# Performance work log

Hardware: AMD Instinct MI355X
Metric: run time of the kernel (lower is better)

## Reference

```python
import jax, jax.numpy as jnp
import numpy as np

S, B, D, H, K, M, MEM = 1024, 2, 1024, 16, 64, 4096, 1
T = (MEM + 1) * S  # key length = (mem_len+1)*seq_len


def setup_inputs() -> dict:
    key = jax.random.key(0)
    ks = jax.random.split(key, 16)

    def w(k, shape):  # N(0, 0.02) init as in the torch module
        return jax.random.normal(k, shape, dtype=jnp.float32) * 0.02

    x = jax.random.normal(ks[0], (S, B, D), dtype=jnp.float32)
    p = jax.random.normal(ks[1], (T, B, D), dtype=jnp.float32)
    memory = jax.random.normal(ks[2], (MEM * S, B, D), dtype=jnp.float32)
    u_bias = w(ks[3], (H, K))
    v_bias = w(ks[4], (H, K))
    # Transformer-XL causal mask: query s may attend to keys t <= mem_len*S + s
    t_idx = jnp.arange(T)[None, :]
    s_idx = jnp.arange(S)[:, None]
    mask = jnp.where(t_idx <= MEM * S + s_idx, 0.0, -1e9).astype(jnp.float32)[None]  # [1,S,T]
    return {
        "x": x, "p": p, "mask": mask, "memory": memory,
        "u_bias": u_bias, "v_bias": v_bias,
        "wq_w": w(ks[5], (H * K, D)), "wke_w": w(ks[6], (H * K, D)),
        "wkr_w": w(ks[7], (H * K, D)), "wv_w": w(ks[8], (H * K, D)),
        "wc_w": w(ks[9], (D, H * K)),
        "w1_w": w(ks[10], (M, D)), "w1_b": jnp.zeros((M,), jnp.float32),
        "w2_w": w(ks[11], (D, M)), "w2_b": jnp.zeros((D,), jnp.float32),
        "ln1_g": jnp.ones((D,), jnp.float32), "ln1_b": jnp.zeros((D,), jnp.float32),
        "ln2_g": jnp.ones((D,), jnp.float32), "ln2_b": jnp.zeros((D,), jnp.float32),
    }


def _layernorm(x, g, b, eps=1e-5):
    mu = jnp.mean(x, axis=-1, keepdims=True)
    var = jnp.mean(jnp.square(x - mu), axis=-1, keepdims=True)
    return (x - mu) / jnp.sqrt(var + eps) * g + b


def reference(x, p, mask, memory, u_bias, v_bias,
              wq_w, wke_w, wkr_w, wv_w, wc_w,
              w1_w, w1_b, w2_w, w2_b, ln1_g, ln1_b, ln2_g, ln2_b):
    s_len, b_sz, d = x.shape
    q = (x @ wq_w.T).reshape(s_len, b_sz, H, K)            # [S,B,H,K]
    x_mem = jnp.concatenate([memory, x], axis=0)           # [T,B,D]
    k_e = (x_mem @ wke_w.T).reshape(T, b_sz, H, K)         # content keys
    k_r = (p @ wkr_w.T).reshape(T, b_sz, H, K)             # relative-position keys
    v = (x_mem @ wv_w.T).reshape(T, b_sz, H, K)
    # AC: content score, BD: relative-position score (Transformer-XL)
    ac = jnp.einsum("sbhk,tbhk->bhst", q + u_bias, k_e)
    bd = jnp.einsum("sbhk,tbhk->bhst", q + v_bias, k_r)
    alpha = (ac + bd) / np.sqrt(K).astype(np.float32) + mask[:, None]  # [B,H,S,T]
    alpha = jax.nn.softmax(alpha, axis=-1)
    av = jnp.einsum("bhst,tbhk->sbhk", alpha, v).reshape(s_len, b_sz, H * K)
    u = av @ wc_w.T
    u = _layernorm(u + x, ln1_g, ln1_b)
    z = jax.nn.relu(u @ w1_w.T + w1_b) @ w2_w.T + w2_b
    z = _layernorm(z + u, ln2_g, ln2_b)
    return z
```

## Files before the change

kernel.cpp:

```cpp
#include <hip/hip_runtime.h>
#include <math.h>

#define S_LEN 1024
#define BATCH 2
#define DM 1024
#define NH 16
#define HD 64
#define FFN_DIM 4096
#define T_LEN 2048
#define RQ 2048
#define RT 4096
#define KROW 72
#define NPART 2

typedef __attribute__((ext_vector_type(8))) short short8;
typedef __attribute__((ext_vector_type(4))) float f32x4;

__device__ __forceinline__ unsigned short f2bf(float f) {
    unsigned u = __builtin_bit_cast(unsigned, f);
    u += 0x7fffu + ((u >> 16) & 1u);
    return (unsigned short)(u >> 16);
}
__device__ __forceinline__ float bf2f(unsigned short s) { return __builtin_bit_cast(float, ((unsigned)s) << 16); }

#define GLD_LDS16(gptr, lptr)                                                                  \
    __builtin_amdgcn_global_load_lds((const __attribute__((address_space(1))) unsigned int*)(gptr), \
                                     (__attribute__((address_space(3))) unsigned int*)(lptr), 16, 0, 0)

__device__ __forceinline__ ushort4 cvt4(float4 v) {
    ushort4 o;
    o.x = f2bf(v.x); o.y = f2bf(v.y); o.z = f2bf(v.z); o.w = f2bf(v.w);
    return o;
}

__global__ void cast_all_kernel(const float* __restrict__ wq, const float* __restrict__ wke,
                                const float* __restrict__ wv, const float* __restrict__ wkr,
                                const float* __restrict__ wc, const float* __restrict__ w1,
                                const float* __restrict__ w2, const float* __restrict__ x,
                                const float* __restrict__ p, const float* __restrict__ mem,
                                unsigned short* __restrict__ wdst, unsigned short* __restrict__ xbf,
                                unsigned short* __restrict__ pbf, unsigned short* __restrict__ xm) {
    const long Q = 256 * 1024;
    const long W = 13 * Q;
    long i = (long)blockIdx.x * blockDim.x + threadIdx.x;
    if (i < W) {
        const float* src; long off;
        if      (i < 1 * Q) { src = wq;  off = 0; }
        else if (i < 2 * Q) { src = wke; off = 1 * Q; }
        else if (i < 3 * Q) { src = wv;  off = 2 * Q; }
        else if (i < 4 * Q) { src = wkr; off = 3 * Q; }
        else if (i < 5 * Q) { src = wc;  off = 4 * Q; }
        else if (i < 9 * Q) { src = w1;  off = 5 * Q; }
        else                { src = w2;  off = 9 * Q; }
        ((ushort4*)wdst)[i] = cvt4(((const float4*)src)[i - off]);
    } else if (i < W + 2 * Q) {
        long j = i - W;
        ((ushort4*)xbf)[j] = cvt4(((const float4*)x)[j]);
    } else if (i < W + 6 * Q) {
        long j = i - W - 2 * Q;
        ((ushort4*)pbf)[j] = cvt4(((const float4*)p)[j]);
    } else {
        long j = i - W - 6 * Q;
        float4 v = (j < 2 * Q) ? ((const float4*)mem)[j] : ((const float4*)x)[j - 2 * Q];
        ((ushort4*)xm)[j] = cvt4(v);
    }
}

#define BM 128
#define BN 128
#define BK 32

__launch_bounds__(256)
__global__ void proj_fused(const unsigned short* __restrict__ xbf, const unsigned short* __restrict__ xmbf,
                           const unsigned short* __restrict__ pbf, const unsigned short* __restrict__ wqb,
                           const unsigned short* __restrict__ wkevb, const unsigned short* __restrict__ wkrb,
                           unsigned short* __restrict__ qo, unsigned short* __restrict__ keo,
                           unsigned short* __restrict__ vTo, unsigned short* __restrict__ kro) {
    __shared__ __align__(16) short As[BM * BK];
    __shared__ __align__(16) short Bs[BN * BK];
    const int id = blockIdx.x;
    const unsigned short *A, *B;
    unsigned short *Yb, *Yv = nullptr;
    int bx, by;
    if (id < 128)      { A = xbf;  B = wqb;   Yb = qo;  bx = id & 7;   by = id >> 3; }
    else if (id < 640) { int t = id - 128; A = xmbf; B = wkevb; Yb = keo; Yv = vTo;
                         bx = t & 15; by = t >> 4; }
    else               { int t = id - 640; A = pbf;  B = wkrb;  Yb = kro;
                         bx = t & 7;  by = t >> 3; }
    const int tid = threadIdx.x;
    const int w = tid >> 6, lane = tid & 63;
    const int row0 = by * BM, col0 = bx * BN;
    const int wr = (w >> 1) * 64, wcn = (w & 1) * 64;
    f32x4 acc[4][4] = {};
    const int lrow = lane & 15, quad = lane >> 4;
    for (int k0 = 0; k0 < DM; k0 += BK) {
        __syncthreads();
#pragma unroll
        for (int i = 0; i < 2; ++i) {
            int c = w * 128 + i * 64 + lane;
            int row = c >> 2, kg = c & 3;
            int kl = (kg - (row >> 1)) & 3;
            GLD_LDS16(A + (long)(row0 + row) * DM + k0 + kl * 8, As + (w * 128 + i * 64) * 8);
            GLD_LDS16(B + (long)(col0 + row) * DM + k0 + kl * 8, Bs + (w * 128 + i * 64) * 8);
        }
        __syncthreads();
        short8 a[4], b[4];
#pragma unroll
        for (int mi = 0; mi < 4; ++mi) {
            int r = wr + mi * 16 + lrow;
            int ph = (quad + (r >> 1)) & 3;
            a[mi] = *(const short8*)&As[r * BK + ph * 8];
        }
#pragma unroll
        for (int ni = 0; ni < 4; ++ni) {
            int r = wcn + ni * 16 + lrow;
            int ph = (quad + (r >> 1)) & 3;
            b[ni] = *(const short8*)&Bs[r * BK + ph * 8];
        }
#pragma unroll
        for (int mi = 0; mi < 4; ++mi)
#pragma unroll
            for (int ni = 0; ni < 4; ++ni)
                acc[mi][ni] = __builtin_amdgcn_mfma_f32_16x16x32_bf16(a[mi], b[ni], acc[mi][ni], 0, 0, 0);
    }
    const int mb = row0 + wr + quad * 4;
    const int nb = col0 + wcn + lrow;
    const bool isv = (Yv != nullptr) && (col0 >= 1024);
#pragma unroll
    for (int mi = 0; mi < 4; ++mi)
#pragma unroll
        for (int ni = 0; ni < 4; ++ni) {
            const int r = mb + mi * 16, cc = nb + ni * 16;
#pragma unroll
            for (int reg = 0; reg < 4; ++reg) {
                float val = acc[mi][ni][reg];
                const int rf = r + reg;
                if (isv) {
                    int c2 = cc - 1024;
                    int t = rf >> 1, b2 = rf & 1;
                    int h2 = c2 >> 6, d2 = c2 & 63;
                    Yv[((long)(b2 * NH + h2) * HD + d2) * T_LEN + t] = f2bf(val);
                } else {
                    Yb[(long)rf * DM + cc] = f2bf(val);
                }
            }
        }
}

__launch_bounds__(256)
__global__ void gemm_mfma(const unsigned short* __restrict__ A, const unsigned short* __restrict__ B,
                          const float* __restrict__ bias, float* __restrict__ Yf,
                          unsigned short* __restrict__ Yb, int Kd, int N, int relu,
                          int klen, long pstride) {
    __shared__ __align__(16) short As[BM * BK];
    __shared__ __align__(16) short Bs[BN * BK];
    const int tid = threadIdx.x;
    const int w = tid >> 6, lane = tid & 63;
    const int row0 = blockIdx.y * BM, col0 = blockIdx.x * BN;
    const int kbeg = blockIdx.z * klen;
    const int wr = (w >> 1) * 64, wcn = (w & 1) * 64;
    f32x4 acc[4][4] = {};
    const int lrow = lane & 15, quad = lane >> 4;
    for (int k0 = kbeg; k0 < kbeg + klen; k0 += BK) {
        __syncthreads();
#pragma unroll
        for (int i = 0; i < 2; ++i) {
            int c = w * 128 + i * 64 + lane;
            int row = c >> 2, kg = c & 3;
            int kl = (kg - (row >> 1)) & 3;
            GLD_LDS16(A + (long)(row0 + row) * Kd + k0 + kl * 8, As + (w * 128 + i * 64) * 8);
            GLD_LDS16(B + (long)(col0 + row) * Kd + k0 + kl * 8, Bs + (w * 128 + i * 64) * 8);
        }
        __syncthreads();
        short8 a[4], b[4];
#pragma unroll
        for (int mi = 0; mi < 4; ++mi) {
            int r = wr + mi * 16 + lrow;
            int ph = (quad + (r >> 1)) & 3;
            a[mi] = *(const short8*)&As[r * BK + ph * 8];
        }
#pragma unroll
        for (int ni = 0; ni < 4; ++ni) {
            int r = wcn + ni * 16 + lrow;
            int ph = (quad + (r >> 1)) & 3;
            b[ni] = *(const short8*)&Bs[r * BK + ph * 8];
        }
#pragma unroll
        for (int mi = 0; mi < 4; ++mi)
#pragma unroll
            for (int ni = 0; ni < 4; ++ni)
                acc[mi][ni] = __builtin_amdgcn_mfma_f32_16x16x32_bf16(a[mi], b[ni], acc[mi][ni], 0, 0, 0);
    }
    const int mb = row0 + wr + quad * 4;
    const int nb = col0 + wcn + lrow;
    float* of = Yf ? Yf + (long)blockIdx.z * pstride : nullptr;
    float bb[4];
#pragma unroll
    for (int ni = 0; ni < 4; ++ni) bb[ni] = bias ? bias[nb + ni * 16] : 0.f;
#pragma unroll
    for (int mi = 0; mi < 4; ++mi)
#pragma unroll
        for (int ni = 0; ni < 4; ++ni) {
            const int r = mb + mi * 16, cc = nb + ni * 16;
#pragma unroll
            for (int reg = 0; reg < 4; ++reg) {
                float val = acc[mi][ni][reg] + bb[ni];
                if (relu) val = fmaxf(val, 0.f);
                if (Yb) Yb[(long)(r + reg) * N + cc] = f2bf(val);
                else    of[(long)(r + reg) * N + cc] = val;
            }
        }
}

__launch_bounds__(256)
__global__ void prep_kernel(const unsigned short* __restrict__ kr,
                            const float* __restrict__ ub, const float* __restrict__ vb,
                            unsigned short* __restrict__ ke_io, float* __restrict__ biasg) {
    const int r = blockIdx.x;
    const int tid = threadIdx.x;
    const int h = tid >> 4, seg = tid & 15;
    ushort4 keu = ((const ushort4*)(ke_io + (long)r * DM))[tid];
    ushort4 kru = ((const ushort4*)(kr + (long)r * DM))[tid];
    float ke0 = bf2f(keu.x), ke1 = bf2f(keu.y), ke2 = bf2f(keu.z), ke3 = bf2f(keu.w);
    float kr0 = bf2f(kru.x), kr1 = bf2f(kru.y), kr2 = bf2f(kru.z), kr3 = bf2f(kru.w);
    float4 u4 = ((const float4*)ub)[tid];
    float4 v4 = ((const float4*)vb)[tid];
    ushort4 s;
    s.x = f2bf((ke0 + kr0) * 0.125f); s.y = f2bf((ke1 + kr1) * 0.125f);
    s.z = f2bf((ke2 + kr2) * 0.125f); s.w = f2bf((ke3 + kr3) * 0.125f);
    ((ushort4*)(ke_io + (long)r * DM))[tid] = s;
    float part = u4.x * ke0 + u4.y * ke1 + u4.z * ke2 + u4.w * ke3
               + v4.x * kr0 + v4.y * kr1 + v4.z * kr2 + v4.w * kr3;
    part += __shfl_xor(part, 1);
    part += __shfl_xor(part, 2);
    part += __shfl_xor(part, 4);
    part += __shfl_xor(part, 8);
    if (seg == 0) {
        const int t = r >> 1, b = r & 1;
        biasg[(b * NH + h) * T_LEN + t] = part * 0.125f;
    }
}

__launch_bounds__(256)
__global__ void attn_mfma(const unsigned short* __restrict__ qg,
                          const unsigned short* __restrict__ ksum,
                          const unsigned short* __restrict__ vT,
                          const float* __restrict__ biasg,
                          float* __restrict__ Opart, float2* __restrict__ mlout) {
    __shared__ __align__(16) unsigned short Ks[64 * KROW];
    __shared__ __align__(16) unsigned short Vs[64 * KROW];
    __shared__ __align__(16) unsigned short Ps[4][16 * KROW];
    const int bid = blockIdx.x;
    const int part = bid >> 9, rid = bid & 511;
    const int stile = rid & 15, h = (rid >> 4) & 15, b = rid >> 8;
    const int tid = threadIdx.x, w = tid >> 6, lane = tid & 63;
    const int L = lane & 15, quad = lane >> 4;
    const int qbase = stile * 64 + w * 16;
    short8 qf0, qf1;
    {
        const unsigned short* qp = qg + ((long)(qbase + L) * 2 + b) * DM + h * HD + quad * 8;
        qf0 = *(const short8*)(qp);
        qf1 = *(const short8*)(qp + 32);
    }
    f32x4 O[4] = {};
    float mrow[4] = {-1e30f, -1e30f, -1e30f, -1e30f};
    float lrow[4] = {0.f, 0.f, 0.f, 0.f};
    const int nch = 17 + stile;
    const float* bias_p = biasg + (long)(b * NH + h) * T_LEN;
    const unsigned short* ks_base = ksum + (long)b * DM + h * HD;
    const unsigned short* vt_base = vT + (long)(b * NH + h) * HD * T_LEN;
    const int c0 = tid, c1 = 256 + tid;
    const int row_a = c0 >> 3, seg_a = c0 & 7;
    const int row_b = c1 >> 3, seg_b = c1 & 7;
    uint4 pk0, pk1, pv0, pv1;
    {
        const int tf = part * 64;
        pk0 = *(const uint4*)(ks_base + (long)(tf + row_a) * 2 * DM + seg_a * 8);
        pk1 = *(const uint4*)(ks_base + (long)(tf + row_b) * 2 * DM + seg_b * 8);
        pv0 = *(const uint4*)(vt_base + (long)row_a * T_LEN + tf + seg_a * 8);
        pv1 = *(const uint4*)(vt_base + (long)row_b * T_LEN + tf + seg_b * 8);
    }
    for (int ch = part; ch < nch; ch += NPART) {
        const int t0 = ch * 64;
        __syncthreads();
        *(uint4*)&Ks[row_a * KROW + seg_a * 8] = pk0;
        *(uint4*)&Ks[row_b * KROW + seg_b * 8] = pk1;
        *(uint4*)&Vs[row_a * KROW + seg_a * 8] = pv0;
        *(uint4*)&Vs[row_b * KROW + seg_b * 8] = pv1;
        __syncthreads();
        if (ch + NPART < nch) {
            const int t1 = t0 + NPART * 64;
            pk0 = *(const uint4*)(ks_base + (long)(t1 + row_a) * 2 * DM + seg_a * 8);
            pk1 = *(const uint4*)(ks_base + (long)(t1 + row_b) * 2 * DM + seg_b * 8);
            pv0 = *(const uint4*)(vt_base + (long)row_a * T_LEN + t1 + seg_a * 8);
            pv1 = *(const uint4*)(vt_base + (long)row_b * T_LEN + t1 + seg_b * 8);
        }
        f32x4 S[4] = {};
#pragma unroll
        for (int kt = 0; kt < 4; ++kt) {
            short8 kb0 = *(const short8*)&Ks[(kt * 16 + L) * KROW + quad * 8];
            short8 kb1 = *(const short8*)&Ks[(kt * 16 + L) * KROW + 32 + quad * 8];
            S[kt] = __builtin_amdgcn_mfma_f32_16x16x32_bf16(qf0, kb0, S[kt], 0, 0, 0);
            S[kt] = __builtin_amdgcn_mfma_f32_16x16x32_bf16(qf1, kb1, S[kt], 0, 0, 0);
        }
        float sc[4][4];
        float cm[4] = {-1e30f, -1e30f, -1e30f, -1e30f};
#pragma unroll
        for (int kt = 0; kt < 4; ++kt) {
            float bt = bias_p[t0 + kt * 16 + L];
#pragma unroll
            for (int reg = 0; reg < 4; ++reg) {
                float v = S[kt][reg] + bt;
                if (t0 + kt * 16 + L > 1024 + qbase + quad * 4 + reg) v = -1e30f;
                sc[kt][reg] = v;
                cm[reg] = fmaxf(cm[reg], v);
            }
        }
#pragma unroll
        for (int off = 1; off < 16; off <<= 1)
#pragma unroll
            for (int reg = 0; reg < 4; ++reg) cm[reg] = fmaxf(cm[reg], __shfl_xor(cm[reg], off));
        float cf[4];
#pragma unroll
        for (int reg = 0; reg < 4; ++reg) {
            float mn = fmaxf(mrow[reg], cm[reg]);
            cf[reg] = __expf(mrow[reg] - mn);
            mrow[reg] = mn;
            lrow[reg] *= cf[reg];
        }
        float rs[4] = {0.f, 0.f, 0.f, 0.f};
#pragma unroll
        for (int kt = 0; kt < 4; ++kt)
#pragma unroll
            for (int reg = 0; reg < 4; ++reg) {
                float pv = __expf(sc[kt][reg] - mrow[reg]);
                rs[reg] += pv;
                Ps[w][(quad * 4 + reg) * KROW + kt * 16 + L] = f2bf(pv);
            }
#pragma unroll
        for (int off = 1; off < 16; off <<= 1)
#pragma unroll
            for (int reg = 0; reg < 4; ++reg) rs[reg] += __shfl_xor(rs[reg], off);
#pragma unroll
        for (int reg = 0; reg < 4; ++reg) lrow[reg] += rs[reg];
#pragma unroll
        for (int dt = 0; dt < 4; ++dt)
#pragma unroll
            for (int reg = 0; reg < 4; ++reg) O[dt][reg] *= cf[reg];
        short8 pa0 = *(const short8*)&Ps[w][L * KROW + quad * 8];
        short8 pa1 = *(const short8*)&Ps[w][L * KROW + 32 + quad * 8];
#pragma unroll
        for (int dt = 0; dt < 4; ++dt) {
            short8 vb0 = *(const short8*)&Vs[(dt * 16 + L) * KROW + quad * 8];
            short8 vb1 = *(const short8*)&Vs[(dt * 16 + L) * KROW + 32 + quad * 8];
            O[dt] = __builtin_amdgcn_mfma_f32_16x16x32_bf16(pa0, vb0, O[dt], 0, 0, 0);
            O[dt] = __builtin_amdgcn_mfma_f32_16x16x32_bf16(pa1, vb1, O[dt], 0, 0, 0);
        }
    }
    const long rbase = ((long)(part * 2 + b) * NH + h) * S_LEN;
#pragma unroll
    for (int reg = 0; reg < 4; ++reg) {
        const int s = qbase + quad * 4 + reg;
        float* op = Opart + (rbase + s) * 64;
#pragma unroll
        for (int dt = 0; dt < 4; ++dt) op[dt * 16 + L] = O[dt][reg];
        if (L == 0) mlout[rbase + s] = make_float2(mrow[reg], lrow[reg]);
    }
}

__launch_bounds__(256)
__global__ void attn_combine(const float* __restrict__ Opart, const float2* __restrict__ ml,
                             unsigned short* __restrict__ avout) {
    const int i = blockIdx.x * 256 + threadIdx.x;
    const int d4 = i & 15;
    const int row = i >> 4;
    const int s = row & 1023;
    const int bh = row >> 10;
    const int b = bh >> 4, h = bh & 15;
    float2 ml0 = ml[row], ml1 = ml[row + 32768];
    float m = fmaxf(ml0.x, ml1.x);
    float a0 = __expf(ml0.x - m), a1 = __expf(ml1.x - m);
    float inv = 1.f / (a0 * ml0.y + a1 * ml1.y);
    a0 *= inv; a1 *= inv;
    float4 o0 = ((const float4*)Opart)[(long)row * 16 + d4];
    float4 o1 = ((const float4*)Opart)[((long)row + 32768) * 16 + d4];
    float4 o;
    o.x = a0 * o0.x + a1 * o1.x;
    o.y = a0 * o0.y + a1 * o1.y;
    o.z = a0 * o0.z + a1 * o1.z;
    o.w = a0 * o0.w + a1 * o1.w;
    *(ushort4*)(avout + ((long)s * 2 + b) * DM + h * HD + d4 * 4) = cvt4(o);
}

__launch_bounds__(256)
__global__ void ln_kernel(const float* __restrict__ a0, const float* __restrict__ a1,
                          const float* __restrict__ cb, const float* __restrict__ r,
                          const float* __restrict__ g, const float* __restrict__ be,
                          float* __restrict__ out, unsigned short* __restrict__ outb) {
    const int row = blockIdx.x;
    const int tid = threadIdx.x;
    float4 xa = ((const float4*)(a0 + (long)row * DM))[tid];
    if (a1) {
        float4 x1 = ((const float4*)(a1 + (long)row * DM))[tid];
        xa.x += x1.x; xa.y += x1.y; xa.z += x1.z; xa.w += x1.w;
    }
    if (cb) {
        float4 c4 = ((const float4*)cb)[tid];
        xa.x += c4.x; xa.y += c4.y; xa.z += c4.z; xa.w += c4.w;
    }
    float4 xr = ((const float4*)(r + (long)row * DM))[tid];
    float4 x = make_float4(xa.x + xr.x, xa.y + xr.y, xa.z + xr.z, xa.w + xr.w);
    float s1 = x.x + x.y + x.z + x.w;
    float s2 = x.x * x.x + x.y * x.y + x.z * x.z + x.w * x.w;
#pragma unroll
    for (int off = 32; off > 0; off >>= 1) {
        s1 += __shfl_down(s1, off);
        s2 += __shfl_down(s2, off);
    }
    __shared__ float w1s[4], w2s[4];
    const int wid = tid >> 6;
    if ((tid & 63) == 0) { w1s[wid] = s1; w2s[wid] = s2; }
    __syncthreads();
    float S1 = w1s[0] + w1s[1] + w1s[2] + w1s[3];
    float S2 = w2s[0] + w2s[1] + w2s[2] + w2s[3];
    float mu = S1 * (1.f / 1024.f);
    float var = S2 * (1.f / 1024.f) - mu * mu;
    float rstd = rsqrtf(var + 1e-5f);
    float4 gv = ((const float4*)g)[tid];
    float4 bv = ((const float4*)be)[tid];
    float4 o;
    o.x = (x.x - mu) * rstd * gv.x + bv.x;
    o.y = (x.y - mu) * rstd * gv.y + bv.y;
    o.z = (x.z - mu) * rstd * gv.z + bv.z;
    o.w = (x.w - mu) * rstd * gv.w + bv.w;
    ((float4*)(out + (long)row * DM))[tid] = o;
    if (outb) ((ushort4*)(outb + (long)row * DM))[tid] = cvt4(o);
}

extern "C" void kernel_launch(void* const* d_in, const int* in_sizes, int n_in,
                              void* d_out, int out_size, void* d_ws, size_t ws_size,
                              hipStream_t stream) {
    (void)in_sizes; (void)n_in; (void)out_size; (void)ws_size;
    const float* x    = (const float*)d_in[0];
    const float* p    = (const float*)d_in[1];
    const float* mem  = (const float*)d_in[3];
    const float* ub   = (const float*)d_in[4];
    const float* vb   = (const float*)d_in[5];
    const float* wq   = (const float*)d_in[6];
    const float* wke  = (const float*)d_in[7];
    const float* wkr  = (const float*)d_in[8];
    const float* wv   = (const float*)d_in[9];
    const float* wc   = (const float*)d_in[10];
    const float* w1   = (const float*)d_in[11];
    const float* w1b  = (const float*)d_in[12];
    const float* w2   = (const float*)d_in[13];
    const float* w2b  = (const float*)d_in[14];
    const float* ln1g = (const float*)d_in[15];
    const float* ln1b = (const float*)d_in[16];
    const float* ln2g = (const float*)d_in[17];
    const float* ln2b = (const float*)d_in[18];
    float* out = (float*)d_out;
    float* wsf = (float*)d_ws;
    unsigned short* ws16 = (unsigned short*)d_ws;

    const long HLF = 512 * 1024;
    const long M16 = 1024 * 1024;
    unsigned short* wq_bf   = ws16 + 0 * M16;
    unsigned short* wkev_bf = ws16 + 1 * M16;
    unsigned short* wkr_bf  = ws16 + 3 * M16;
    unsigned short* wc_bf   = ws16 + 4 * M16;
    unsigned short* w1_bf   = ws16 + 5 * M16;
    unsigned short* w2_bf   = ws16 + 9 * M16;
    unsigned short* x_bf   = (unsigned short*)(wsf + 13 * HLF);
    unsigned short* xm_bf  = (unsigned short*)(wsf + 15 * HLF);
    unsigned short* p_bf   = (unsigned short*)(wsf + 19 * HLF);
    unsigned short* q_bf   = (unsigned short*)(wsf + 23 * HLF);
    unsigned short* ke_bf  = (unsigned short*)(wsf + 25 * HLF);
    unsigned short* kr_bf  = (unsigned short*)(wsf + 29 * HLF);
    unsigned short* vT_bf  = (unsigned short*)(wsf + 33 * HLF);
    float* abias           = wsf + 37 * HLF;
    float* Opart           = wsf + 15 * HLF;
    float2* mlpart         = (float2*)(wsf + 29 * HLF);
    unsigned short* avb_bf = (unsigned short*)(wsf + 13 * HLF);
    float* t1p             = wsf + 15 * HLF;
    float* u               = wsf + 25 * HLF;
    unsigned short* u_bf   = (unsigned short*)(wsf + 23 * HLF);
    unsigned short* z1_bf  = (unsigned short*)(wsf + 15 * HLF);
    float* t2p             = wsf + 29 * HLF;
    const long PSTR = (long)2048 * 1024;

    cast_all_kernel<<<23552, 256, 0, stream>>>(wq, wke, wv, wkr, wc, w1, w2, x, p, mem,
                                               ws16, x_bf, p_bf, xm_bf);
    proj_fused<<<896, 256, 0, stream>>>(x_bf, xm_bf, p_bf, wq_bf, wkev_bf, wkr_bf,
                                        q_bf, ke_bf, vT_bf, kr_bf);
    prep_kernel<<<RT, 256, 0, stream>>>(kr_bf, ub, vb, ke_bf, abias);
    attn_mfma<<<512 * NPART, 256, 0, stream>>>(q_bf, ke_bf, vT_bf, abias, Opart, mlpart);
    attn_combine<<<2048, 256, 0, stream>>>(Opart, mlpart, avb_bf);
    gemm_mfma<<<dim3(8, 16, 2), 256, 0, stream>>>(avb_bf, wc_bf, nullptr, t1p, nullptr,
                                                  DM, DM, 0, 512, PSTR);
    ln_kernel<<<RQ, 256, 0, stream>>>(t1p, t1p + PSTR, nullptr, x, ln1g, ln1b, u, u_bf);
    gemm_mfma<<<dim3(32, 16, 1), 256, 0, stream>>>(u_bf, w1_bf, w1b, nullptr, z1_bf,
                                                   DM, FFN_DIM, 1, DM, 0);
    gemm_mfma<<<dim3(8, 16, 2), 256, 0, stream>>>(z1_bf, w2_bf, nullptr, t2p, nullptr,
                                                  FFN_DIM, DM, 0, 2048, PSTR);
    ln_kernel<<<RQ, 256, 0, stream>>>(t2p, t2p + PSTR, w2b, u, ln2g, ln2b, out, nullptr);
}
```

Baseline: 406.8 us.

## Split attention key range three ways, prefetch bias, mask only final chunk

The attention kernel now splits each query tile's key chunks across three partitions instead of two, launching more blocks to improve GPU fill and load balance across the causal-length tiles. The combine kernel merges three partial softmax results, and workspace buffers are re-laid out so the extra partial output fits. The per-chunk bias load is prefetched one iteration ahead together with K/V, and the causal mask compare runs only on the diagonal chunk. In exchange, the extra partition writes and reads more partial output and adds one more exp and rescale per row in the combine step.

Result: no change. 402.3 us (-1.1%).

```diff
diff --git a/kernel.cpp b/kernel.cpp
--- a/kernel.cpp
+++ b/kernel.cpp
@@ -11,7 +11,8 @@
 #define RQ 2048
 #define RT 4096
 #define KROW 72
-#define NPART 2
+#define NPART 3
+#define OPSTR 2097152L
 
 typedef __attribute__((ext_vector_type(8))) short short8;
 typedef __attribute__((ext_vector_type(4))) float f32x4;
@@ -246,7 +247,8 @@
                           const unsigned short* __restrict__ ksum,
                           const unsigned short* __restrict__ vT,
                           const float* __restrict__ biasg,
-                          float* __restrict__ Opart, float2* __restrict__ mlout) {
+                          float* __restrict__ Op01, float* __restrict__ Op2,
+                          float2* __restrict__ mlout) {
     __shared__ __align__(16) unsigned short Ks[64 * KROW];
     __shared__ __align__(16) unsigned short Vs[64 * KROW];
     __shared__ __align__(16) unsigned short Ps[4][16 * KROW];
@@ -273,12 +275,15 @@
     const int row_a = c0 >> 3, seg_a = c0 & 7;
     const int row_b = c1 >> 3, seg_b = c1 & 7;
     uint4 pk0, pk1, pv0, pv1;
+    float pb[4];
     {
         const int tf = part * 64;
         pk0 = *(const uint4*)(ks_base + (long)(tf + row_a) * 2 * DM + seg_a * 8);
         pk1 = *(const uint4*)(ks_base + (long)(tf + row_b) * 2 * DM + seg_b * 8);
         pv0 = *(const uint4*)(vt_base + (long)row_a * T_LEN + tf + seg_a * 8);
         pv1 = *(const uint4*)(vt_base + (long)row_b * T_LEN + tf + seg_b * 8);
+#pragma unroll
+        for (int kt = 0; kt < 4; ++kt) pb[kt] = bias_p[tf + kt * 16 + L];
     }
     for (int ch = part; ch < nch; ch += NPART) {
         const int t0 = ch * 64;
@@ -288,12 +293,16 @@
         *(uint4*)&Vs[row_a * KROW + seg_a * 8] = pv0;
         *(uint4*)&Vs[row_b * KROW + seg_b * 8] = pv1;
         __syncthreads();
-        if (ch + NPART < nch) {
+        const bool more = (ch + NPART < nch);
+        float pbn[4];
+        if (more) {
             const int t1 = t0 + NPART * 64;
             pk0 = *(const uint4*)(ks_base + (long)(t1 + row_a) * 2 * DM + seg_a * 8);
             pk1 = *(const uint4*)(ks_base + (long)(t1 + row_b) * 2 * DM + seg_b * 8);
             pv0 = *(const uint4*)(vt_base + (long)row_a * T_LEN + t1 + seg_a * 8);
             pv1 = *(const uint4*)(vt_base + (long)row_b * T_LEN + t1 + seg_b * 8);
+#pragma unroll
+            for (int kt = 0; kt < 4; ++kt) pbn[kt] = bias_p[t1 + kt * 16 + L];
         }
         f32x4 S[4] = {};
 #pragma unroll
@@ -305,16 +314,25 @@
         }
         float sc[4][4];
         float cm[4] = {-1e30f, -1e30f, -1e30f, -1e30f};
-#pragma unroll
-        for (int kt = 0; kt < 4; ++kt) {
-            float bt = bias_p[t0 + kt * 16 + L];
-#pragma unroll
-            for (int reg = 0; reg < 4; ++reg) {
-                float v = S[kt][reg] + bt;
-                if (t0 + kt * 16 + L > 1024 + qbase + quad * 4 + reg) v = -1e30f;
-                sc[kt][reg] = v;
-                cm[reg] = fmaxf(cm[reg], v);
-            }
+        if (ch != nch - 1) {
+#pragma unroll
+            for (int kt = 0; kt < 4; ++kt)
+#pragma unroll
+                for (int reg = 0; reg < 4; ++reg) {
+                    float v = S[kt][reg] + pb[kt];
+                    sc[kt][reg] = v;
+                    cm[reg] = fmaxf(cm[reg], v);
+                }
+        } else {
+#pragma unroll
+            for (int kt = 0; kt < 4; ++kt)
+#pragma unroll
+                for (int reg = 0; reg < 4; ++reg) {
+                    float v = S[kt][reg] + pb[kt];
+                    if (t0 + kt * 16 + L > 1024 + qbase + quad * 4 + reg) v = -1e30f;
+                    sc[kt][reg] = v;
+                    cm[reg] = fmaxf(cm[reg], v);
+                }
         }
 #pragma unroll
         for (int off = 1; off < 16; off <<= 1)
@@ -356,20 +374,26 @@
             O[dt] = __builtin_amdgcn_mfma_f32_16x16x32_bf16(pa0, vb0, O[dt], 0, 0, 0);
             O[dt] = __builtin_amdgcn_mfma_f32_16x16x32_bf16(pa1, vb1, O[dt], 0, 0, 0);
         }
-    }
-    const long rbase = ((long)(part * 2 + b) * NH + h) * S_LEN;
+        if (more) {
+#pragma unroll
+            for (int kt = 0; kt < 4; ++kt) pb[kt] = pbn[kt];
+        }
+    }
+    float* ob = (part < 2) ? Op01 + (long)part * OPSTR : Op2;
+    const long rbase = ((long)b * NH + h) * S_LEN;
 #pragma unroll
     for (int reg = 0; reg < 4; ++reg) {
         const int s = qbase + quad * 4 + reg;
-        float* op = Opart + (rbase + s) * 64;
+        float* op = ob + (rbase + s) * 64;
 #pragma unroll
         for (int dt = 0; dt < 4; ++dt) op[dt * 16 + L] = O[dt][reg];
-        if (L == 0) mlout[rbase + s] = make_float2(mrow[reg], lrow[reg]);
+        if (L == 0) mlout[(long)part * 32768 + rbase + s] = make_float2(mrow[reg], lrow[reg]);
     }
 }
 
 __launch_bounds__(256)
-__global__ void attn_combine(const float* __restrict__ Opart, const float2* __restrict__ ml,
+__global__ void attn_combine(const float* __restrict__ Op01, const float* __restrict__ Op2,
+                             const float2* __restrict__ ml,
                              unsigned short* __restrict__ avout) {
     const int i = blockIdx.x * 256 + threadIdx.x;
     const int d4 = i & 15;
@@ -377,18 +401,19 @@
     const int s = row & 1023;
     const int bh = row >> 10;
     const int b = bh >> 4, h = bh & 15;
-    float2 ml0 = ml[row], ml1 = ml[row + 32768];
-    float m = fmaxf(ml0.x, ml1.x);
-    float a0 = __expf(ml0.x - m), a1 = __expf(ml1.x - m);
-    float inv = 1.f / (a0 * ml0.y + a1 * ml1.y);
-    a0 *= inv; a1 *= inv;
-    float4 o0 = ((const float4*)Opart)[(long)row * 16 + d4];
-    float4 o1 = ((const float4*)Opart)[((long)row + 32768) * 16 + d4];
+    float2 m0 = ml[row], m1 = ml[row + 32768], m2 = ml[row + 65536];
+    float m = fmaxf(fmaxf(m0.x, m1.x), m2.x);
+    float a0 = __expf(m0.x - m), a1 = __expf(m1.x - m), a2 = __expf(m2.x - m);
+    float inv = 1.f / (a0 * m0.y + a1 * m1.y + a2 * m2.y);
+    a0 *= inv; a1 *= inv; a2 *= inv;
+    float4 o0 = ((const float4*)Op01)[(long)row * 16 + d4];
+    float4 o1 = ((const float4*)Op01)[((long)row + 32768) * 16 + d4];
+    float4 o2 = ((const float4*)Op2)[(long)row * 16 + d4];
     float4 o;
-    o.x = a0 * o0.x + a1 * o1.x;
-    o.y = a0 * o0.y + a1 * o1.y;
-    o.z = a0 * o0.z + a1 * o1.z;
-    o.w = a0 * o0.w + a1 * o1.w;
+    o.x = a0 * o0.x + a1 * o1.x + a2 * o2.x;
+    o.y = a0 * o0.y + a1 * o1.y + a2 * o2.y;
+    o.z = a0 * o0.z + a1 * o1.z + a2 * o2.z;
+    o.w = a0 * o0.w + a1 * o1.w + a2 * o2.w;
     *(ushort4*)(avout + ((long)s * 2 + b) * DM + h * HD + d4 * 4) = cvt4(o);
 }
 
@@ -479,13 +504,14 @@
     unsigned short* kr_bf  = (unsigned short*)(wsf + 29 * HLF);
     unsigned short* vT_bf  = (unsigned short*)(wsf + 33 * HLF);
     float* abias           = wsf + 37 * HLF;
-    float* Opart           = wsf + 15 * HLF;
-    float2* mlpart         = (float2*)(wsf + 29 * HLF);
-    unsigned short* avb_bf = (unsigned short*)(wsf + 13 * HLF);
+    float2* mlpart         = (float2*)(wsf + 13 * HLF);
+    float* Op01            = wsf + 15 * HLF;
+    float* Op2             = wsf + 29 * HLF;
+    unsigned short* avb_bf = (unsigned short*)(wsf + 33 * HLF);
     float* t1p             = wsf + 15 * HLF;
     float* u               = wsf + 25 * HLF;
     unsigned short* u_bf   = (unsigned short*)(wsf + 23 * HLF);
-    unsigned short* z1_bf  = (unsigned short*)(wsf + 15 * HLF);
+    unsigned short* z1_bf  = (unsigned short*)(wsf + 13 * HLF);
     float* t2p             = wsf + 29 * HLF;
     const long PSTR = (long)2048 * 1024;
 
@@ -494,8 +520,8 @@
     proj_fused<<<896, 256, 0, stream>>>(x_bf, xm_bf, p_bf, wq_bf, wkev_bf, wkr_bf,
                                         q_bf, ke_bf, vT_bf, kr_bf);
     prep_kernel<<<RT, 256, 0, stream>>>(kr_bf, ub, vb, ke_bf, abias);
-    attn_mfma<<<512 * NPART, 256, 0, stream>>>(q_bf, ke_bf, vT_bf, abias, Opart, mlpart);
-    attn_combine<<<2048, 256, 0, stream>>>(Opart, mlpart, avb_bf);
+    attn_mfma<<<512 * NPART, 256, 0, stream>>>(q_bf, ke_bf, vT_bf, abias, Op01, Op2, mlpart);
+    attn_combine<<<2048, 256, 0, stream>>>(Op01, Op2, mlpart, avb_bf);
     gemm_mfma<<<dim3(8, 16, 2), 256, 0, stream>>>(avb_bf, wc_bf, nullptr, t1p, nullptr,
                                                   DM, DM, 0, 512, PSTR);
     ln_kernel<<<RQ, 256, 0, stream>>>(t1p, t1p + PSTR, nullptr, x, ln1g, ln1b, u, u_bf);
```
